# Performance work log

Hardware: AMD Instinct MI355X
Metric: run time of the kernel (lower is better)

## Reference

```python
import jax, jax.numpy as jnp
import numpy as np

DIM = 1024
SEQ_LEN = 4096
K = 256
HEADS = 16
DIM_HEAD = DIM // HEADS  # 64
BATCH = 4


def setup_inputs() -> dict:
    key = jax.random.key(0)
    ks = jax.random.split(key, 8)
    x = jax.random.normal(ks[0], (BATCH, SEQ_LEN, DIM), dtype=jnp.float32)
    # nn.Linear weights are [out, in]; y = x @ W.T
    std_lin = 1.0 / np.sqrt(DIM)
    Wq = jax.random.uniform(ks[1], (HEADS * DIM_HEAD, DIM), minval=-std_lin, maxval=std_lin, dtype=jnp.float32)
    Wk = jax.random.uniform(ks[2], (HEADS * DIM_HEAD, DIM), minval=-std_lin, maxval=std_lin, dtype=jnp.float32)
    Wv = jax.random.uniform(ks[3], (HEADS * DIM_HEAD, DIM), minval=-std_lin, maxval=std_lin, dtype=jnp.float32)
    # proj_k/proj_v init_: uniform(-1/sqrt(k), 1/sqrt(k)) on [seq_len, k]
    std_p = 1.0 / np.sqrt(K)
    proj_k = jax.random.uniform(ks[4], (SEQ_LEN, K), minval=-std_p, maxval=std_p, dtype=jnp.float32)
    proj_v = jax.random.uniform(ks[5], (SEQ_LEN, K), minval=-std_p, maxval=std_p, dtype=jnp.float32)
    std_o = 1.0 / np.sqrt(HEADS * DIM_HEAD)
    Wo = jax.random.uniform(ks[6], (DIM, HEADS * DIM_HEAD), minval=-std_o, maxval=std_o, dtype=jnp.float32)
    bo = jax.random.uniform(ks[7], (DIM,), minval=-std_o, maxval=std_o, dtype=jnp.float32)
    return {"x": x, "Wq": Wq, "Wk": Wk, "Wv": Wv, "proj_k": proj_k, "proj_v": proj_v, "Wo": Wo, "bo": bo}


def reference(x, Wq, Wk, Wv, proj_k, proj_v, Wo, bo):
    b, n, d = x.shape
    h, dh, k = HEADS, DIM_HEAD, K
    # q/k/v projections
    q = jnp.einsum('bnd,ed->bne', x, Wq)            # [b, n, h*dh]
    keys = jnp.einsum('bnd,ed->bne', x, Wk)         # [b, n, h*dh]
    vals = jnp.einsum('bnd,ed->bne', x, Wv)         # [b, n, h*dh]
    # low-rank projection along sequence: [b, n, e] x [n, k] -> [b, k, e]
    keys = jnp.einsum('bne,nk->bke', keys, proj_k[:n])
    vals = jnp.einsum('bne,nk->bke', vals, proj_v[:n])
    # split heads
    q = q.reshape(b, n, h, dh).transpose(0, 2, 1, 3)        # [b, h, n, dh]
    keys = keys.reshape(b, k, h, dh).transpose(0, 2, 1, 3)  # [b, h, k, dh]
    vals = vals.reshape(b, k, h, dh).transpose(0, 2, 1, 3)  # [b, h, k, dh]
    dots = jnp.einsum('bhnd,bhkd->bhnk', q, keys) * (dh ** -0.5)
    attn = jax.nn.softmax(dots, axis=-1)
    out = jnp.einsum('bhnk,bhkd->bhnd', attn, vals)
    out = out.transpose(0, 2, 1, 3).reshape(b, n, h * dh)
    return jnp.einsum('bne,oe->bno', out, Wo) + bo
```

## Files before the change

kernel.cpp:

```cpp
#include <hip/hip_runtime.h>
#include <hip/hip_bf16.h>
#include <stdint.h>

typedef unsigned short u16;
typedef __attribute__((ext_vector_type(8))) short bf16x8;
typedef __attribute__((ext_vector_type(4))) float f32x4;

#define DEV __device__ __forceinline__

DEV u16 f2bf(float f) {
  union { float f; unsigned u; } v; v.f = f;
  unsigned r = (v.u + 0x7fffu + ((v.u >> 16) & 1u)) >> 16;
  return (u16)r;
}

DEV f32x4 mfma16(bf16x8 a, bf16x8 b, f32x4 c) {
  return __builtin_amdgcn_mfma_f32_16x16x32_bf16(a, b, c, 0, 0, 0);
}

DEV void gload_lds16(const u16* g, u16* l) {
  __builtin_amdgcn_global_load_lds((const __attribute__((address_space(1))) void*)g,
                                   (__attribute__((address_space(3))) void*)l, 16, 0, 0);
}

__global__ void cvt_xpose_kernel(const float* __restrict__ src, u16* __restrict__ dst_rm,
                                 u16* __restrict__ dst_tp, int R, int C,
                                 long zS, long zRM, long zTP) {
  __shared__ u16 tile[64][72];
  src += (size_t)blockIdx.z * zS;
  dst_tp += (size_t)blockIdx.z * zTP;
  int r0 = blockIdx.y * 64, c0 = blockIdx.x * 64;
  int tr = threadIdx.x >> 2, tc = (threadIdx.x & 3) * 16;
  const float* s = src + (size_t)(r0 + tr) * C + c0 + tc;
  u16 loc[16];
#pragma unroll
  for (int q = 0; q < 4; ++q) {
    float4 v = ((const float4*)s)[q];
    loc[q * 4 + 0] = f2bf(v.x); loc[q * 4 + 1] = f2bf(v.y);
    loc[q * 4 + 2] = f2bf(v.z); loc[q * 4 + 3] = f2bf(v.w);
  }
#pragma unroll
  for (int i = 0; i < 16; ++i) tile[tr][tc + i] = loc[i];
  if (dst_rm) {
    u16* d = dst_rm + (size_t)blockIdx.z * zRM + (size_t)(r0 + tr) * C + c0 + tc;
    *(bf16x8*)d = *(const bf16x8*)&loc[0];
    *(bf16x8*)(d + 8) = *(const bf16x8*)&loc[8];
  }
  __syncthreads();
  u16 tmp[16];
#pragma unroll
  for (int i = 0; i < 16; ++i) tmp[i] = tile[tc + i][tr];
  u16* d = dst_tp + (size_t)(c0 + tr) * R + r0 + tc;
  *(bf16x8*)d = *(const bf16x8*)&tmp[0];
  *(bf16x8*)(d + 8) = *(const bf16x8*)&tmp[8];
}

__global__ void cvt_w4_kernel(const float* __restrict__ s0, const float* __restrict__ s1,
                              const float* __restrict__ s2, const float* __restrict__ s3,
                              u16* __restrict__ d0, u16* __restrict__ d1,
                              u16* __restrict__ d2, u16* __restrict__ d3) {
  const float* s; u16* d;
  switch (blockIdx.y) {
    case 0: s = s0; d = d0; break;
    case 1: s = s1; d = d1; break;
    case 2: s = s2; d = d2; break;
    default: s = s3; d = d3; break;
  }
  int i = blockIdx.x * 256 + threadIdx.x;
  float4 v = ((const float4*)s)[i];
  ushort4 o; o.x = f2bf(v.x); o.y = f2bf(v.y); o.z = f2bf(v.z); o.w = f2bf(v.w);
  ((ushort4*)d)[i] = o;
}

__global__ void reduce4_kernel(const float* __restrict__ part, u16* __restrict__ out) {
  int i = blockIdx.x * 256 + threadIdx.x;
  const float4* p = (const float4*)part;
  float4 a = p[i], b = p[i + 524288], c = p[i + 1048576], d = p[i + 1572864];
  ushort4 o;
  o.x = f2bf(a.x + b.x + c.x + d.x);
  o.y = f2bf(a.y + b.y + c.y + d.y);
  o.z = f2bf(a.z + b.z + c.z + d.z);
  o.w = f2bf(a.w + b.w + c.w + d.w);
  ((ushort4*)out)[i] = o;
}

template<int OMODE>
__global__ __launch_bounds__(256, 3)
void gemm_bt_kernel(const u16* __restrict__ A, const u16* __restrict__ Bt,
                    const u16* __restrict__ Bt2, void* __restrict__ Cout,
                    const float* __restrict__ bias,
                    int ldA, int ldB, int ldC, int Klen,
                    long zA, long zB, long zC, int bMod, long kChunk) {
  __shared__ __align__(16) u16 smA[2][128 * 32];
  __shared__ __align__(16) u16 smB[2][128 * 32];
  const int t = threadIdx.x;
  const int lane = t & 63, wave = t >> 6;
  const int wm = wave & 1, wn = wave >> 1;
  const int g = lane >> 4, r = lane & 15;
  const int id = (blockIdx.y << 3) | blockIdx.x;
  const int s = (id & 7) * gridDim.y + (id >> 3);
  const int bx = s & 7, by = s >> 3;
  const int z = blockIdx.z;
  const int b = z % bMod, kc = z / bMod;
  const u16* Ab = A + (size_t)b * zA + (size_t)kc * kChunk;
  const u16* Bbase = (Bt2 && (b & 1)) ? Bt2 : Bt;
  const u16* Bb = Bbase + (size_t)b * zB + (size_t)kc * kChunk;
  const int m0 = by * 128, n0 = bx * 128;
  const int srow = t >> 2;
  const int lslot = ((t & 3) + 4 - ((srow >> 1) & 3)) & 3;

  f32x4 acc[4][4];
#pragma unroll
  for (int m = 0; m < 4; ++m)
#pragma unroll
    for (int n = 0; n < 4; ++n) acc[m][n] = f32x4{0.f, 0.f, 0.f, 0.f};

  auto STAGE = [&](int buf, int k0) {
#pragma unroll
    for (int p = 0; p < 2; ++p) {
      int row = p * 64 + srow;
      gload_lds16(Ab + (size_t)(m0 + row) * ldA + k0 + lslot * 8, &smA[buf][p * 2048 + wave * 512]);
      gload_lds16(Bb + (size_t)(n0 + row) * ldB + k0 + lslot * 8, &smB[buf][p * 2048 + wave * 512]);
    }
  };

  const int nt = Klen >> 5;
  STAGE(0, 0);
  __syncthreads();
  int cur = 0;
  for (int it = 0; it < nt; ++it) {
    if (it + 1 < nt) STAGE(cur ^ 1, (it + 1) << 5);
    bf16x8 af[4], bfr[4];
#pragma unroll
    for (int m = 0; m < 4; ++m) {
      int row = wm * 64 + m * 16 + r;
      int ps = (g + (row >> 1)) & 3;
      af[m] = *(const bf16x8*)&smA[cur][row * 32 + ps * 8];
    }
#pragma unroll
    for (int n = 0; n < 4; ++n) {
      int row = wn * 64 + n * 16 + r;
      int ps = (g + (row >> 1)) & 3;
      bfr[n] = *(const bf16x8*)&smB[cur][row * 32 + ps * 8];
    }
#pragma unroll
    for (int m = 0; m < 4; ++m)
#pragma unroll
      for (int n = 0; n < 4; ++n)
        acc[m][n] = mfma16(af[m], bfr[n], acc[m][n]);
    __syncthreads();
    cur ^= 1;
  }

  if constexpr (OMODE == 0) {
    u16* C = (u16*)Cout + (size_t)z * zC;
#pragma unroll
    for (int n = 0; n < 4; ++n) {
      int col = n0 + wn * 64 + n * 16 + r;
#pragma unroll
      for (int m = 0; m < 4; ++m) {
        int rowb = m0 + wm * 64 + m * 16 + 4 * g;
#pragma unroll
        for (int rr = 0; rr < 4; ++rr)
          C[(size_t)(rowb + rr) * ldC + col] = f2bf(acc[m][n][rr]);
      }
    }
  } else {
    float* C = (float*)Cout + (size_t)z * zC;
#pragma unroll
    for (int n = 0; n < 4; ++n) {
      int col = n0 + wn * 64 + n * 16 + r;
      float bv = (OMODE == 1) ? bias[col] : 0.f;
#pragma unroll
      for (int m = 0; m < 4; ++m) {
        int rowb = m0 + wm * 64 + m * 16 + 4 * g;
#pragma unroll
        for (int rr = 0; rr < 4; ++rr)
          C[(size_t)(rowb + rr) * ldC + col] = acc[m][n][rr] + bv;
      }
    }
  }
}

__global__ __launch_bounds__(256, 2)
void attn_kernel(const u16* __restrict__ Q, const u16* __restrict__ Kl,
                 const u16* __restrict__ Vl, u16* __restrict__ Out) {
  __shared__ __align__(16) u16 smKV[256 * 64];
  __shared__ __align__(16) u16 smP[64 * 256];
  const int t = threadIdx.x, lane = t & 63, w = t >> 6;
  const int g = lane >> 4, r = lane & 15;
  const int id = (blockIdx.y << 6) | blockIdx.x;
  const int s = (id & 7) * (gridDim.y << 3) + (id >> 3);
  const int b = blockIdx.z, h = s >> 6, n0 = (s & 63) * 64;
  const u16* Kb = Kl + (size_t)b * 524288 + h * 64;
  const u16* Vb = Vl + (size_t)b * 524288 + h * 64;

#pragma unroll
  for (int p = 0; p < 8; ++p) {
    int row = p * 32 + (t >> 3);
    int ls = ((t & 7) + 8 - (row & 7)) & 7;
    gload_lds16(Kb + (size_t)row * 1024 + ls * 8, smKV + p * 2048 + w * 512);
  }
  int qrow = n0 + w * 16 + r;
  const u16* Qp = Q + ((size_t)(b * 4096 + qrow)) * 1024 + h * 64 + g * 8;
  bf16x8 aq0 = *(const bf16x8*)Qp;
  bf16x8 aq1 = *(const bf16x8*)(Qp + 32);
  __syncthreads();

  f32x4 dotv[16];
#pragma unroll
  for (int kf = 0; kf < 16; ++kf) {
    int row = kf * 16 + r;
    bf16x8 kb0 = *(const bf16x8*)&smKV[row * 64 + ((g + row) & 7) * 8];
    bf16x8 kb1 = *(const bf16x8*)&smKV[row * 64 + ((4 + g + row) & 7) * 8];
    f32x4 d = f32x4{0.f, 0.f, 0.f, 0.f};
    d = mfma16(aq0, kb0, d);
    d = mfma16(aq1, kb1, d);
    dotv[kf] = d;
  }

  float rsum[4];
#pragma unroll
  for (int rr = 0; rr < 4; ++rr) {
    float m = dotv[0][rr];
#pragma unroll
    for (int kf = 1; kf < 16; ++kf) m = fmaxf(m, dotv[kf][rr]);
#pragma unroll
    for (int mask = 1; mask < 16; mask <<= 1) m = fmaxf(m, __shfl_xor(m, mask, 64));
    int prow = w * 16 + 4 * g + rr;
    float ssum = 0.f;
#pragma unroll
    for (int kf = 0; kf < 16; ++kf) {
      float p = __expf((dotv[kf][rr] - m) * 0.125f);
      ssum += p;
      int idx = (prow * 256 + kf * 16 + r) ^ ((prow & 7) << 3);
      smP[idx] = f2bf(p);
    }
#pragma unroll
    for (int mask = 1; mask < 16; mask <<= 1) ssum += __shfl_xor(ssum, mask, 64);
    rsum[rr] = 1.f / ssum;
  }
  __syncthreads();

  {
    int k = t;
#pragma unroll
    for (int c8 = 0; c8 < 8; ++c8) {
      bf16x8 v = *(const bf16x8*)(Vb + (size_t)k * 1024 + c8 * 8);
#pragma unroll
      for (int j = 0; j < 8; ++j) {
        int d = c8 * 8 + j;
        int idx = (d * 256 + k) ^ ((d & 7) << 3);
        smKV[idx] = (u16)v[j];
      }
    }
  }
  __syncthreads();

  f32x4 oacc[4];
#pragma unroll
  for (int df = 0; df < 4; ++df) oacc[df] = f32x4{0.f, 0.f, 0.f, 0.f};
#pragma unroll
  for (int kk = 0; kk < 8; ++kk) {
    int prow = w * 16 + r;
    bf16x8 ap = *(const bf16x8*)&smP[(prow * 256 + kk * 32 + g * 8) ^ ((prow & 7) << 3)];
#pragma unroll
    for (int df = 0; df < 4; ++df) {
      int vrow = df * 16 + r;
      bf16x8 bv = *(const bf16x8*)&smKV[(vrow * 256 + kk * 32 + g * 8) ^ ((vrow & 7) << 3)];
      oacc[df] = mfma16(ap, bv, oacc[df]);
    }
  }
#pragma unroll
  for (int df = 0; df < 4; ++df)
#pragma unroll
    for (int rr = 0; rr < 4; ++rr) {
      int orow = n0 + w * 16 + 4 * g + rr;
      int ocol = h * 64 + df * 16 + r;
      Out[((size_t)(b * 4096 + orow)) * 1024 + ocol] = f2bf(oacc[df][rr] * rsum[rr]);
    }
}

extern "C" void kernel_launch(void* const* d_in, const int* in_sizes, int n_in,
                              void* d_out, int out_size, void* d_ws, size_t ws_size,
                              hipStream_t stream) {
  const float* x  = (const float*)d_in[0];
  const float* Wq = (const float*)d_in[1];
  const float* Wk = (const float*)d_in[2];
  const float* Wv = (const float*)d_in[3];
  const float* pk = (const float*)d_in[4];
  const float* pv = (const float*)d_in[5];
  const float* Wo = (const float*)d_in[6];
  const float* bo = (const float*)d_in[7];

  u16* ws = (u16*)d_ws;
  u16* xbf   = ws;
  u16* xT    = xbf + 16777216;
  u16* wqb   = xT + 16777216;
  u16* wkb   = wqb + 1048576;
  u16* wvb   = wkb + 1048576;
  u16* wob   = wvb + 1048576;
  u16* projT = wob + 1048576;
  u16* Qb    = projT + 2097152;
  u16* xp    = Qb + 16777216;
  u16* kvlow = xp + 2097152;
  u16* aout  = xbf;
  float* xp_part = (float*)Qb;

  cvt_xpose_kernel<<<dim3(16, 64, 4), 256, 0, stream>>>(x, xbf, xT, 4096, 1024,
                                                        4194304, 4194304, 4194304);
  cvt_w4_kernel<<<dim3(1024, 4), 256, 0, stream>>>(Wq, Wk, Wv, Wo, wqb, wkb, wvb, wob);
  cvt_xpose_kernel<<<dim3(4, 64, 1), 256, 0, stream>>>(pk, nullptr, projT, 4096, 256, 0, 0, 0);
  cvt_xpose_kernel<<<dim3(4, 64, 1), 256, 0, stream>>>(pv, nullptr, projT + 1048576, 4096, 256, 0, 0, 0);
  gemm_bt_kernel<2><<<dim3(8, 4, 16), 256, 0, stream>>>(
      projT, xT, nullptr, (void*)xp_part, nullptr,
      4096, 4096, 1024, 1024, 0, 4194304, 524288, 4, 1024);
  reduce4_kernel<<<2048, 256, 0, stream>>>(xp_part, xp);
  gemm_bt_kernel<0><<<dim3(8, 2, 8), 256, 0, stream>>>(
      xp, wkb, wvb, (void*)kvlow, nullptr,
      1024, 1024, 1024, 1024, 262144, 0, 262144, 8, 0);
  gemm_bt_kernel<0><<<dim3(8, 128, 1), 256, 0, stream>>>(
      xbf, wqb, nullptr, (void*)Qb, nullptr,
      1024, 1024, 1024, 1024, 0, 0, 0, 1, 0);
  attn_kernel<<<dim3(64, 16, 4), 256, 0, stream>>>(Qb, kvlow, kvlow + 262144, aout);
  gemm_bt_kernel<1><<<dim3(8, 128, 1), 256, 0, stream>>>(
      aout, wob, nullptr, d_out, bo,
      1024, 1024, 1024, 1024, 0, 0, 0, 1, 0);
}
```

Measured before the change: 242.0 us.

## Pre-transpose V in the KV GEMM and fold softmax scale into Q

The K/V projection GEMM now writes V transposed into a separate buffer, and the Q GEMM pre-multiplies by log2(e)/sqrt(dh), so the attention kernel can use exp2 directly. The attention kernel drops the LDS transpose of V and its extra barrier, reading V^T fragments straight from global memory. It also swaps MFMA operand order so each lane holds a full score row, which makes the softmax reductions cheaper. Normalised probabilities reuse a single shared buffer, which halves LDS use and lets occupancy rise to three blocks. The cost is uncoalesced-ish global V reads per wave and strided transposed stores in the GEMM epilogue.

Result: slower. 256.5 us (+6.0%).

```diff
diff --git a/kernel.cpp b/kernel.cpp
--- a/kernel.cpp
+++ b/kernel.cpp
@@ -22,6 +22,8 @@
   __builtin_amdgcn_global_load_lds((const __attribute__((address_space(1))) void*)g,
                                    (__attribute__((address_space(3))) void*)l, 16, 0, 0);
 }
+
+#define QSCALE 0.18033688011112042f
 
 __global__ void cvt_xpose_kernel(const float* __restrict__ src, u16* __restrict__ dst_rm,
                                  u16* __restrict__ dst_tp, int R, int C,
@@ -88,7 +90,7 @@
 __global__ __launch_bounds__(256, 3)
 void gemm_bt_kernel(const u16* __restrict__ A, const u16* __restrict__ Bt,
                     const u16* __restrict__ Bt2, void* __restrict__ Cout,
-                    const float* __restrict__ bias,
+                    u16* __restrict__ CoutT, const float* __restrict__ bias, float cscale,
                     int ldA, int ldB, int ldC, int Klen,
                     long zA, long zB, long zC, int bMod, long kChunk) {
   __shared__ __align__(16) u16 smA[2][128 * 32];
@@ -162,7 +164,36 @@
         int rowb = m0 + wm * 64 + m * 16 + 4 * g;
 #pragma unroll
         for (int rr = 0; rr < 4; ++rr)
-          C[(size_t)(rowb + rr) * ldC + col] = f2bf(acc[m][n][rr]);
+          C[(size_t)(rowb + rr) * ldC + col] = f2bf(acc[m][n][rr] * cscale);
+      }
+    }
+  } else if constexpr (OMODE == 3) {
+    if ((z & 1) == 0) {
+      u16* C = (u16*)Cout + (size_t)(z >> 1) * zC;
+#pragma unroll
+      for (int n = 0; n < 4; ++n) {
+        int col = n0 + wn * 64 + n * 16 + r;
+#pragma unroll
+        for (int m = 0; m < 4; ++m) {
+          int rowb = m0 + wm * 64 + m * 16 + 4 * g;
+#pragma unroll
+          for (int rr = 0; rr < 4; ++rr)
+            C[(size_t)(rowb + rr) * ldC + col] = f2bf(acc[m][n][rr]);
+        }
+      }
+    } else {
+      u16* C = CoutT + (size_t)(z >> 1) * zC;
+#pragma unroll
+      for (int n = 0; n < 4; ++n) {
+        int col = n0 + wn * 64 + n * 16 + r;
+#pragma unroll
+        for (int m = 0; m < 4; ++m) {
+          int rowb = m0 + wm * 64 + m * 16 + 4 * g;
+          ushort4 o;
+          o.x = f2bf(acc[m][n][0]); o.y = f2bf(acc[m][n][1]);
+          o.z = f2bf(acc[m][n][2]); o.w = f2bf(acc[m][n][3]);
+          *(ushort4*)&C[(size_t)col * 256 + rowb] = o;
+        }
       }
     }
   } else {
@@ -182,26 +213,25 @@
   }
 }
 
-__global__ __launch_bounds__(256, 2)
+__global__ __launch_bounds__(256, 3)
 void attn_kernel(const u16* __restrict__ Q, const u16* __restrict__ Kl,
-                 const u16* __restrict__ Vl, u16* __restrict__ Out) {
-  __shared__ __align__(16) u16 smKV[256 * 64];
-  __shared__ __align__(16) u16 smP[64 * 256];
+                 const u16* __restrict__ VT, u16* __restrict__ Out) {
+  __shared__ __align__(16) u16 sm[256 * 64];
   const int t = threadIdx.x, lane = t & 63, w = t >> 6;
   const int g = lane >> 4, r = lane & 15;
   const int id = (blockIdx.y << 6) | blockIdx.x;
   const int s = (id & 7) * (gridDim.y << 3) + (id >> 3);
   const int b = blockIdx.z, h = s >> 6, n0 = (s & 63) * 64;
-  const u16* Kb = Kl + (size_t)b * 524288 + h * 64;
-  const u16* Vb = Vl + (size_t)b * 524288 + h * 64;
+  const u16* Kb = Kl + (size_t)b * 262144 + h * 64;
+  const u16* Vb = VT + (size_t)b * 262144 + (size_t)(h * 64) * 256;
 
 #pragma unroll
   for (int p = 0; p < 8; ++p) {
     int row = p * 32 + (t >> 3);
     int ls = ((t & 7) + 8 - (row & 7)) & 7;
-    gload_lds16(Kb + (size_t)row * 1024 + ls * 8, smKV + p * 2048 + w * 512);
-  }
-  int qrow = n0 + w * 16 + r;
+    gload_lds16(Kb + (size_t)row * 1024 + ls * 8, sm + p * 2048 + w * 512);
+  }
+  const int qrow = n0 + w * 16 + r;
   const u16* Qp = Q + ((size_t)(b * 4096 + qrow)) * 1024 + h * 64 + g * 8;
   bf16x8 aq0 = *(const bf16x8*)Qp;
   bf16x8 aq1 = *(const bf16x8*)(Qp + 32);
@@ -211,63 +241,53 @@
 #pragma unroll
   for (int kf = 0; kf < 16; ++kf) {
     int row = kf * 16 + r;
-    bf16x8 kb0 = *(const bf16x8*)&smKV[row * 64 + ((g + row) & 7) * 8];
-    bf16x8 kb1 = *(const bf16x8*)&smKV[row * 64 + ((4 + g + row) & 7) * 8];
+    bf16x8 kb0 = *(const bf16x8*)&sm[row * 64 + ((g + row) & 7) * 8];
+    bf16x8 kb1 = *(const bf16x8*)&sm[row * 64 + ((4 + g + row) & 7) * 8];
     f32x4 d = f32x4{0.f, 0.f, 0.f, 0.f};
-    d = mfma16(aq0, kb0, d);
-    d = mfma16(aq1, kb1, d);
+    d = mfma16(kb0, aq0, d);
+    d = mfma16(kb1, aq1, d);
     dotv[kf] = d;
   }
-
-  float rsum[4];
-#pragma unroll
-  for (int rr = 0; rr < 4; ++rr) {
-    float m = dotv[0][rr];
-#pragma unroll
-    for (int kf = 1; kf < 16; ++kf) m = fmaxf(m, dotv[kf][rr]);
-#pragma unroll
-    for (int mask = 1; mask < 16; mask <<= 1) m = fmaxf(m, __shfl_xor(m, mask, 64));
-    int prow = w * 16 + 4 * g + rr;
-    float ssum = 0.f;
-#pragma unroll
-    for (int kf = 0; kf < 16; ++kf) {
-      float p = __expf((dotv[kf][rr] - m) * 0.125f);
+  __syncthreads();
+
+  float mx = -3.4e38f;
+#pragma unroll
+  for (int kf = 0; kf < 16; ++kf)
+    mx = fmaxf(mx, fmaxf(fmaxf(dotv[kf][0], dotv[kf][1]), fmaxf(dotv[kf][2], dotv[kf][3])));
+  mx = fmaxf(mx, __shfl_xor(mx, 16, 64));
+  mx = fmaxf(mx, __shfl_xor(mx, 32, 64));
+  float ssum = 0.f;
+#pragma unroll
+  for (int kf = 0; kf < 16; ++kf)
+#pragma unroll
+    for (int j = 0; j < 4; ++j) {
+      float p = exp2f(dotv[kf][j] - mx);
+      dotv[kf][j] = p;
       ssum += p;
-      int idx = (prow * 256 + kf * 16 + r) ^ ((prow & 7) << 3);
-      smP[idx] = f2bf(p);
-    }
-#pragma unroll
-    for (int mask = 1; mask < 16; mask <<= 1) ssum += __shfl_xor(ssum, mask, 64);
-    rsum[rr] = 1.f / ssum;
-  }
-  __syncthreads();
-
-  {
-    int k = t;
-#pragma unroll
-    for (int c8 = 0; c8 < 8; ++c8) {
-      bf16x8 v = *(const bf16x8*)(Vb + (size_t)k * 1024 + c8 * 8);
-#pragma unroll
-      for (int j = 0; j < 8; ++j) {
-        int d = c8 * 8 + j;
-        int idx = (d * 256 + k) ^ ((d & 7) << 3);
-        smKV[idx] = (u16)v[j];
-      }
-    }
-  }
-  __syncthreads();
+    }
+  ssum += __shfl_xor(ssum, 16, 64);
+  ssum += __shfl_xor(ssum, 32, 64);
+  const float inv = 1.f / ssum;
+
+  const int q16 = w * 16 + r;
+  const int qx = (q16 & 7) << 3;
+#pragma unroll
+  for (int kf = 0; kf < 16; ++kf) {
+    ushort4 pk;
+    pk.x = f2bf(dotv[kf][0] * inv); pk.y = f2bf(dotv[kf][1] * inv);
+    pk.z = f2bf(dotv[kf][2] * inv); pk.w = f2bf(dotv[kf][3] * inv);
+    *(ushort4*)&sm[(q16 * 256 + kf * 16 + 4 * g) ^ qx] = pk;
+  }
 
   f32x4 oacc[4];
 #pragma unroll
   for (int df = 0; df < 4; ++df) oacc[df] = f32x4{0.f, 0.f, 0.f, 0.f};
 #pragma unroll
   for (int kk = 0; kk < 8; ++kk) {
-    int prow = w * 16 + r;
-    bf16x8 ap = *(const bf16x8*)&smP[(prow * 256 + kk * 32 + g * 8) ^ ((prow & 7) << 3)];
+    bf16x8 ap = *(const bf16x8*)&sm[(q16 * 256 + kk * 32 + g * 8) ^ qx];
 #pragma unroll
     for (int df = 0; df < 4; ++df) {
-      int vrow = df * 16 + r;
-      bf16x8 bv = *(const bf16x8*)&smKV[(vrow * 256 + kk * 32 + g * 8) ^ ((vrow & 7) << 3)];
+      bf16x8 bv = *(const bf16x8*)(Vb + (size_t)(df * 16 + r) * 256 + kk * 32 + g * 8);
       oacc[df] = mfma16(ap, bv, oacc[df]);
     }
   }
@@ -277,7 +297,7 @@
     for (int rr = 0; rr < 4; ++rr) {
       int orow = n0 + w * 16 + 4 * g + rr;
       int ocol = h * 64 + df * 16 + r;
-      Out[((size_t)(b * 4096 + orow)) * 1024 + ocol] = f2bf(oacc[df][rr] * rsum[rr]);
+      Out[((size_t)(b * 4096 + orow)) * 1024 + ocol] = f2bf(oacc[df][rr]);
     }
 }
 
@@ -303,7 +323,8 @@
   u16* projT = wob + 1048576;
   u16* Qb    = projT + 2097152;
   u16* xp    = Qb + 16777216;
-  u16* kvlow = xp + 2097152;
+  u16* klow  = xp + 2097152;
+  u16* vT    = klow + 1048576;
   u16* aout  = xbf;
   float* xp_part = (float*)Qb;
 
@@ -313,17 +334,17 @@
   cvt_xpose_kernel<<<dim3(4, 64, 1), 256, 0, stream>>>(pk, nullptr, projT, 4096, 256, 0, 0, 0);
   cvt_xpose_kernel<<<dim3(4, 64, 1), 256, 0, stream>>>(pv, nullptr, projT + 1048576, 4096, 256, 0, 0, 0);
   gemm_bt_kernel<2><<<dim3(8, 4, 16), 256, 0, stream>>>(
-      projT, xT, nullptr, (void*)xp_part, nullptr,
+      projT, xT, nullptr, (void*)xp_part, nullptr, nullptr, 1.f,
       4096, 4096, 1024, 1024, 0, 4194304, 524288, 4, 1024);
   reduce4_kernel<<<2048, 256, 0, stream>>>(xp_part, xp);
-  gemm_bt_kernel<0><<<dim3(8, 2, 8), 256, 0, stream>>>(
-      xp, wkb, wvb, (void*)kvlow, nullptr,
+  gemm_bt_kernel<3><<<dim3(8, 2, 8), 256, 0, stream>>>(
+      xp, wkb, wvb, (void*)klow, vT, nullptr, 1.f,
       1024, 1024, 1024, 1024, 262144, 0, 262144, 8, 0);
   gemm_bt_kernel<0><<<dim3(8, 128, 1), 256, 0, stream>>>(
-      xbf, wqb, nullptr, (void*)Qb, nullptr,
+      xbf, wqb, nullptr, (void*)Qb, nullptr, nullptr, QSCALE,
       1024, 1024, 1024, 1024, 0, 0, 0, 1, 0);
-  attn_kernel<<<dim3(64, 16, 4), 256, 0, stream>>>(Qb, kvlow, kvlow + 262144, aout);
+  attn_kernel<<<dim3(64, 16, 4), 256, 0, stream>>>(Qb, klow, vT, aout);
   gemm_bt_kernel<1><<<dim3(8, 128, 1), 256, 0, stream>>>(
-      aout, wob, nullptr, d_out, bo,
+      aout, wob, nullptr, d_out, nullptr, bo, 1.f,
       1024, 1024, 1024, 1024, 0, 0, 0, 1, 0);
 }
```
